# Kernel optimization log

Hardware: AMD Instinct MI355X
Metric: run time of the kernel (lower is better)

Reference implementation:

```python
import jax, jax.numpy as jnp
import numpy as np

SIZE = 4096  # core_size(16) ** nr_cores(3)


def setup_inputs() -> dict:
    key = jax.random.key(0)
    k_x, k0, k1, k2, kb = jax.random.split(key, 5)
    d, r = 16, 64
    # std per TT.init_core: sigma = (t * sqrt(r)**(1-c))**(1/c), t=1/sqrt(size), c=3
    t = 1.0 / np.sqrt(SIZE)
    sigma = float((t * np.sqrt(r) ** (1 - 3)) ** (1.0 / 3))
    x = jax.random.normal(k_x, (4, 2048, SIZE), dtype=jnp.float32)
    g0 = sigma * jax.random.normal(k0, (1, d, d, r), dtype=jnp.float32)
    g1 = sigma * jax.random.normal(k1, (r, d, d, r), dtype=jnp.float32)
    g2 = sigma * jax.random.normal(k2, (r, d, d, 1), dtype=jnp.float32)
    bias = np.sqrt(1.0 / SIZE) * jax.random.uniform(kb, (SIZE,), dtype=jnp.float32, minval=-1.0, maxval=1.0)
    return {"x": x, "g0": g0, "g1": g1, "g2": g2, "bias": bias}


def reference(x, g0, g1, g2, bias):
    # to_matrix: chain of einsum contractions over TT cores
    G = g0[0]  # (d, d, r)
    G = jnp.einsum('ija,aklb->ijklb', G, g1)      # (d,d,d,d,r)
    G = jnp.einsum('ijkla,amnb->ijklmnb', G, g2)  # (d,d,d,d,d,d,1)
    G = G.reshape(SIZE, SIZE)
    # forward: flatten leading dims, dense matmul + bias, restore shape
    X = x.reshape(-1, SIZE)
    out = X @ G + bias
    return out.reshape(*x.shape[:-1], SIZE)
```

## Files before the change

kernel.cpp:

```cpp
#include <hip/hip_runtime.h>
#include <stdint.h>

#define DI __device__ __forceinline__

using floatx4 = __attribute__((ext_vector_type(4))) float;
using short8  = __attribute__((ext_vector_type(8))) short;

DI uint16_t f2b(float f) {
  uint32_t u = __float_as_uint(f);
  return (uint16_t)((u + 0x7FFFu + ((u >> 16) & 1u)) >> 16);
}

DI void async_cp16(const uint16_t* g, uint16_t* l) {
  __builtin_amdgcn_global_load_lds(
      (const __attribute__((address_space(1))) void*)g,
      (__attribute__((address_space(3))) void*)l, 16, 0, 0);
}

__global__ __launch_bounds__(256)
void cvt_bf16(const float* __restrict__ x, uint16_t* __restrict__ y) {
  long i = ((long)blockIdx.x * 256 + threadIdx.x) * 8;
  float4 a = *(const float4*)(x + i);
  float4 b = *(const float4*)(x + i + 4);
  union { uint16_t u[8]; uint4 v; } o;
  o.u[0] = f2b(a.x); o.u[1] = f2b(a.y); o.u[2] = f2b(a.z); o.u[3] = f2b(a.w);
  o.u[4] = f2b(b.x); o.u[5] = f2b(b.y); o.u[6] = f2b(b.z); o.u[7] = f2b(b.w);
  *(uint4*)(y + i) = o.v;
}

__global__ __launch_bounds__(256)
void tt_t1(const float* __restrict__ g0, const float* __restrict__ g1,
           uint16_t* __restrict__ t1) {
  __shared__ float g0s[64 * 64];
  __shared__ float g1s[64 * 128];
  const int rowbase = blockIdx.x * 64;
  const int colbase = blockIdx.y * 128;
  const int t = threadIdx.x;

  for (int f = t; f < 4096; f += 256) g0s[f] = g0[rowbase * 64 + f];
  for (int f = t; f < 8192; f += 256) {
    int a = f >> 7, c = f & 127;
    g1s[f] = g1[(long)a * 16384 + colbase + c];
  }
  __syncthreads();

  const int tx = t & 31;
  const int ty = t >> 5;
  const int c0 = tx * 4;
  const int r0 = ty * 8;

  float acc[8][4];
  #pragma unroll
  for (int r = 0; r < 8; ++r)
    #pragma unroll
    for (int c = 0; c < 4; ++c) acc[r][c] = 0.f;

  for (int a4 = 0; a4 < 16; ++a4) {
    float g0r[8][4];
    #pragma unroll
    for (int r = 0; r < 8; ++r)
      *(float4*)&g0r[r][0] = *(const float4*)&g0s[(r0 + r) * 64 + a4 * 4];
    #pragma unroll
    for (int e = 0; e < 4; ++e) {
      float4 bv4 = *(const float4*)&g1s[(a4 * 4 + e) * 128 + c0];
      float bv[4] = {bv4.x, bv4.y, bv4.z, bv4.w};
      #pragma unroll
      for (int r = 0; r < 8; ++r)
        #pragma unroll
        for (int c = 0; c < 4; ++c)
          acc[r][c] += g0r[r][e] * bv[c];
    }
  }

  #pragma unroll
  for (int r = 0; r < 8; ++r) {
    ushort4 o;
    o.x = f2b(acc[r][0]); o.y = f2b(acc[r][1]);
    o.z = f2b(acc[r][2]); o.w = f2b(acc[r][3]);
    *(ushort4*)&t1[(long)(rowbase + r0 + r) * 16384 + colbase + c0] = o;
  }
}

__global__ __launch_bounds__(256)
void transpose_t1(const uint16_t* __restrict__ src, uint16_t* __restrict__ dst,
                  const float* __restrict__ g2, uint16_t* __restrict__ g2t) {
  __shared__ uint16_t tile[64][68];
  const int cb = blockIdx.x * 64;
  const int rb = blockIdx.y * 64;
  const int t = threadIdx.x;

  if (blockIdx.y == 0) {
    #pragma unroll
    for (int p = 0; p < 4; ++p) {
      int f = blockIdx.x * 1024 + p * 256 + t;
      int mn = f >> 6, b = f & 63;
      g2t[f] = f2b(g2[b * 256 + mn]);
    }
  }
  {
    const int c4 = (t & 15) * 4;
    const int r  = t >> 4;
    #pragma unroll
    for (int p = 0; p < 4; ++p) {
      int rr = r + p * 16;
      *(ushort4*)&tile[rr][c4] = *(const ushort4*)&src[(long)(rb + rr) * 1024 + cb + c4];
    }
  }
  __syncthreads();
  {
    const int r4 = (t & 15) * 4;
    const int c  = t >> 4;
    #pragma unroll
    for (int p = 0; p < 4; ++p) {
      int cc = c + p * 16;
      ushort4 o;
      o.x = tile[r4 + 0][cc]; o.y = tile[r4 + 1][cc];
      o.z = tile[r4 + 2][cc]; o.w = tile[r4 + 3][cc];
      *(ushort4*)&dst[(long)(cb + cc) * 4096 + rb + r4] = o;
    }
  }
}

#define VSTRIDE 136
__global__ __launch_bounds__(256, 2)
void gemm_fused(const uint16_t* __restrict__ A,
                const uint16_t* __restrict__ Bt,
                const uint16_t* __restrict__ g2t,
                const float* __restrict__ bias,
                float* __restrict__ out) {
  __shared__ __align__(16) uint16_t As[128 * 32];
  __shared__ __align__(16) uint16_t Bs[128 * 32];
  __shared__ __align__(16) uint16_t Vs[128 * VSTRIDE];

  const int bm = blockIdx.x * 128;
  const int bn = blockIdx.y * 128;
  const int tid  = threadIdx.x;
  const int wave = tid >> 6;
  const int lane = tid & 63;
  const int wm = (wave >> 1) * 64;
  const int wn = (wave & 1) * 64;

  const uint16_t* Ab = A + (long)bm * 4096;
  const uint16_t* Bb = Bt + (long)bn * 4096;

  const int srow = lane >> 2;
  const int scol = (lane & 3) * 8;

  floatx4 acc[4][4];
  #pragma unroll
  for (int i = 0; i < 4; ++i)
    #pragma unroll
    for (int j = 0; j < 4; ++j)
      acc[i][j] = (floatx4){0.f, 0.f, 0.f, 0.f};

  const int fr = lane & 15;
  const int fk = (lane >> 4) * 8;

  for (int k0 = 0; k0 < 4096; k0 += 32) {
    __syncthreads();
    #pragma unroll
    for (int t = 0; t < 2; ++t) {
      const int rblk = wave * 2 + t;
      async_cp16(Ab + (long)(rblk * 16 + srow) * 4096 + k0 + scol, &As[rblk * 16 * 32]);
      async_cp16(Bb + (long)(rblk * 16 + srow) * 4096 + k0 + scol, &Bs[rblk * 16 * 32]);
    }
    __syncthreads();

    short8 af[4], bg[4];
    #pragma unroll
    for (int i = 0; i < 4; ++i)
      af[i] = *(const short8*)&As[(wm + i * 16 + fr) * 32 + fk];
    #pragma unroll
    for (int j = 0; j < 4; ++j)
      bg[j] = *(const short8*)&Bs[(wn + j * 16 + fr) * 32 + fk];

    #pragma unroll
    for (int i = 0; i < 4; ++i)
      #pragma unroll
      for (int j = 0; j < 4; ++j)
        acc[i][j] = __builtin_amdgcn_mfma_f32_16x16x32_bf16(af[i], bg[j], acc[i][j], 0, 0, 0);
  }

  const int colq = lane & 15;
  const int rowq = (lane >> 4) * 4;
  __syncthreads();
  #pragma unroll
  for (int i = 0; i < 4; ++i)
    #pragma unroll
    for (int j = 0; j < 4; ++j)
      #pragma unroll
      for (int r = 0; r < 4; ++r)
        Vs[(wm + i * 16 + rowq + r) * VSTRIDE + wn + j * 16 + colq] = f2b(acc[i][j][r]);
  __syncthreads();

  const int bsel   = (wave >> 1) * 64;
  const int mnBase = (wave & 1) * 128;
  const long ocol0 = (long)blockIdx.y * 512 + (wave >> 1) * 256 + mnBase;

  short8 bg2[8][2];
  #pragma unroll
  for (int jn = 0; jn < 8; ++jn)
    #pragma unroll
    for (int ks = 0; ks < 2; ++ks)
      bg2[jn][ks] = *(const short8*)&g2t[(mnBase + jn * 16 + fr) * 64 + ks * 32 + fk];

  float bvs[8];
  #pragma unroll
  for (int jn = 0; jn < 8; ++jn)
    bvs[jn] = bias[ocol0 + jn * 16 + colq];

  #pragma unroll
  for (int pass = 0; pass < 4; ++pass) {
    floatx4 acc2[2][8];
    #pragma unroll
    for (int im = 0; im < 2; ++im)
      #pragma unroll
      for (int jn = 0; jn < 8; ++jn)
        acc2[im][jn] = (floatx4){0.f, 0.f, 0.f, 0.f};

    short8 af2[2][2];
    #pragma unroll
    for (int im = 0; im < 2; ++im)
      #pragma unroll
      for (int ks = 0; ks < 2; ++ks)
        af2[im][ks] = *(const short8*)&Vs[(pass * 32 + im * 16 + fr) * VSTRIDE + bsel + ks * 32 + fk];

    #pragma unroll
    for (int im = 0; im < 2; ++im)
      #pragma unroll
      for (int jn = 0; jn < 8; ++jn)
        #pragma unroll
        for (int ks = 0; ks < 2; ++ks)
          acc2[im][jn] = __builtin_amdgcn_mfma_f32_16x16x32_bf16(af2[im][ks], bg2[jn][ks], acc2[im][jn], 0, 0, 0);

    #pragma unroll
    for (int jn = 0; jn < 8; ++jn)
      #pragma unroll
      for (int im = 0; im < 2; ++im)
        #pragma unroll
        for (int r = 0; r < 4; ++r) {
          const int row = bm + pass * 32 + im * 16 + rowq + r;
          out[(long)row * 4096 + ocol0 + jn * 16 + colq] = acc2[im][jn][r] + bvs[jn];
        }
  }
}

static constexpr long XBF_OFF = 0;
static constexpr long T1_OFF  = 67108864;
static constexpr long T1T_OFF = 75497472;
static constexpr long G2T_OFF = 83886080;

extern "C" void kernel_launch(void* const* d_in, const int* in_sizes, int n_in,
                              void* d_out, int out_size, void* d_ws, size_t ws_size,
                              hipStream_t stream) {
  const float* x    = (const float*)d_in[0];
  const float* g0   = (const float*)d_in[1];
  const float* g1   = (const float*)d_in[2];
  const float* g2   = (const float*)d_in[3];
  const float* bias = (const float*)d_in[4];
  float* out = (float*)d_out;

  char* ws = (char*)d_ws;
  uint16_t* Xbf = (uint16_t*)(ws + XBF_OFF);
  uint16_t* T1  = (uint16_t*)(ws + T1_OFF);
  uint16_t* T1t = (uint16_t*)(ws + T1T_OFF);
  uint16_t* G2T = (uint16_t*)(ws + G2T_OFF);

  cvt_bf16<<<16384, 256, 0, stream>>>(x, Xbf);
  tt_t1<<<dim3(4, 128), 256, 0, stream>>>(g0, g1, T1);
  transpose_t1<<<dim3(16, 64), 256, 0, stream>>>(T1, T1t, g2, G2T);
  gemm_fused<<<dim3(64, 8), 256, 0, stream>>>(Xbf, T1t, G2T, bias, out);
}
```

Before: 350.6 us.

## Double-buffer GEMM mainloop with K=64 stages and a shared LDS pool

Rewrites the GEMM main loop to use two LDS buffers, each holding a K=64 slice of A and B. The async global-to-LDS copy for the next slice is issued before computing on the current one. This halves the number of barriers per K step and overlaps loads with MFMA work. The stage buffers and the epilogue V tile are aliased in one 64KB LDS array, which keeps LDS use near the original and may preserve two blocks per CU.

Result: faster. 335.0 us (-4.5%).

```diff
diff --git a/kernel.cpp b/kernel.cpp
--- a/kernel.cpp
+++ b/kernel.cpp
@@ -122,15 +122,46 @@
 }
 
 #define VSTRIDE 136
+
+DI void compute_half(const uint16_t* __restrict__ as_, const uint16_t* __restrict__ bs_,
+                     int wm, int wn, int fr, int fk, floatx4 acc[4][4]) {
+  short8 af[4], bg[4];
+  #pragma unroll
+  for (int i = 0; i < 4; ++i)
+    af[i] = *(const short8*)&as_[(wm + i * 16 + fr) * 32 + fk];
+  #pragma unroll
+  for (int j = 0; j < 4; ++j)
+    bg[j] = *(const short8*)&bs_[(wn + j * 16 + fr) * 32 + fk];
+  #pragma unroll
+  for (int i = 0; i < 4; ++i)
+    #pragma unroll
+    for (int j = 0; j < 4; ++j)
+      acc[i][j] = __builtin_amdgcn_mfma_f32_16x16x32_bf16(af[i], bg[j], acc[i][j], 0, 0, 0);
+}
+
+DI void stage_tile(const uint16_t* __restrict__ Ab, const uint16_t* __restrict__ Bb,
+                   uint16_t* dstbuf, int k0, int wave, int srow, int scol) {
+  #pragma unroll
+  for (int ks = 0; ks < 2; ++ks)
+    #pragma unroll
+    for (int t = 0; t < 2; ++t) {
+      const int rblk = wave * 2 + t;
+      async_cp16(Ab + (long)(rblk * 16 + srow) * 4096 + k0 + ks * 32 + scol,
+                 dstbuf + ks * 4096 + rblk * 16 * 32);
+      async_cp16(Bb + (long)(rblk * 16 + srow) * 4096 + k0 + ks * 32 + scol,
+                 dstbuf + 8192 + ks * 4096 + rblk * 16 * 32);
+    }
+}
+
 __global__ __launch_bounds__(256, 2)
 void gemm_fused(const uint16_t* __restrict__ A,
                 const uint16_t* __restrict__ Bt,
                 const uint16_t* __restrict__ g2t,
                 const float* __restrict__ bias,
                 float* __restrict__ out) {
-  __shared__ __align__(16) uint16_t As[128 * 32];
-  __shared__ __align__(16) uint16_t Bs[128 * 32];
-  __shared__ __align__(16) uint16_t Vs[128 * VSTRIDE];
+  __shared__ __align__(16) uint16_t lds[32768];
+  uint16_t* buf0 = lds;
+  uint16_t* buf1 = lds + 16384;
 
   const int bm = blockIdx.x * 128;
   const int bn = blockIdx.y * 128;
@@ -145,6 +176,8 @@
 
   const int srow = lane >> 2;
   const int scol = (lane & 3) * 8;
+  const int fr = lane & 15;
+  const int fk = (lane >> 4) * 8;
 
   floatx4 acc[4][4];
   #pragma unroll
@@ -153,33 +186,26 @@
     for (int j = 0; j < 4; ++j)
       acc[i][j] = (floatx4){0.f, 0.f, 0.f, 0.f};
 
-  const int fr = lane & 15;
-  const int fk = (lane >> 4) * 8;
-
-  for (int k0 = 0; k0 < 4096; k0 += 32) {
+  stage_tile(Ab, Bb, buf0, 0, wave, srow, scol);
+  __syncthreads();
+
+  for (int t = 0; t < 62; t += 2) {
+    stage_tile(Ab, Bb, buf1, (t + 1) * 64, wave, srow, scol);
+    compute_half(buf0,        buf0 + 8192,  wm, wn, fr, fk, acc);
+    compute_half(buf0 + 4096, buf0 + 12288, wm, wn, fr, fk, acc);
     __syncthreads();
-    #pragma unroll
-    for (int t = 0; t < 2; ++t) {
-      const int rblk = wave * 2 + t;
-      async_cp16(Ab + (long)(rblk * 16 + srow) * 4096 + k0 + scol, &As[rblk * 16 * 32]);
-      async_cp16(Bb + (long)(rblk * 16 + srow) * 4096 + k0 + scol, &Bs[rblk * 16 * 32]);
-    }
+
+    stage_tile(Ab, Bb, buf0, (t + 2) * 64, wave, srow, scol);
+    compute_half(buf1,        buf1 + 8192,  wm, wn, fr, fk, acc);
+    compute_half(buf1 + 4096, buf1 + 12288, wm, wn, fr, fk, acc);
     __syncthreads();
-
-    short8 af[4], bg[4];
-    #pragma unroll
-    for (int i = 0; i < 4; ++i)
-      af[i] = *(const short8*)&As[(wm + i * 16 + fr) * 32 + fk];
-    #pragma unroll
-    for (int j = 0; j < 4; ++j)
-      bg[j] = *(const short8*)&Bs[(wn + j * 16 + fr) * 32 + fk];
-
-    #pragma unroll
-    for (int i = 0; i < 4; ++i)
-      #pragma unroll
-      for (int j = 0; j < 4; ++j)
-        acc[i][j] = __builtin_amdgcn_mfma_f32_16x16x32_bf16(af[i], bg[j], acc[i][j], 0, 0, 0);
-  }
+  }
+  stage_tile(Ab, Bb, buf1, 63 * 64, wave, srow, scol);
+  compute_half(buf0,        buf0 + 8192,  wm, wn, fr, fk, acc);
+  compute_half(buf0 + 4096, buf0 + 12288, wm, wn, fr, fk, acc);
+  __syncthreads();
+  compute_half(buf1,        buf1 + 8192,  wm, wn, fr, fk, acc);
+  compute_half(buf1 + 4096, buf1 + 12288, wm, wn, fr, fk, acc);
 
   const int colq = lane & 15;
   const int rowq = (lane >> 4) * 4;
@@ -190,7 +216,7 @@
     for (int j = 0; j < 4; ++j)
       #pragma unroll
       for (int r = 0; r < 4; ++r)
-        Vs[(wm + i * 16 + rowq + r) * VSTRIDE + wn + j * 16 + colq] = f2b(acc[i][j][r]);
+        lds[(wm + i * 16 + rowq + r) * VSTRIDE + wn + j * 16 + colq] = f2b(acc[i][j][r]);
   __syncthreads();
 
   const int bsel   = (wave >> 1) * 64;
@@ -223,7 +249,7 @@
     for (int im = 0; im < 2; ++im)
       #pragma unroll
       for (int ks = 0; ks < 2; ++ks)
-        af2[im][ks] = *(const short8*)&Vs[(pass * 32 + im * 16 + fr) * VSTRIDE + bsel + ks * 32 + fk];
+        af2[im][ks] = *(const short8*)&lds[(pass * 32 + im * 16 + fr) * VSTRIDE + bsel + ks * 32 + fk];
 
     #pragma unroll
     for (int im = 0; im < 2; ++im)
```

## Rewrite fused GEMM with 256x128 tiles, triple-buffered async loads and swizzled LDS

Applied to the files above, without the earlier changes.

The main GEMM now uses 512-thread blocks covering 256x128 output tiles with K-steps of 64. Operands are loaded into LDS through a three-buffer async pipeline, using an XOR swizzle to avoid bank conflicts. MFMA work is split into quads interleaved with prefetch, barriers and setprio. The epilogue also uses the swizzled layout, with 8 waves each computing a 64-column slice of the second contraction. This aims to hide global-load latency behind compute and reduce per-iteration barrier stalls, at the cost of about 144KB of dynamic LDS and higher register pressure, which limits occupancy.

New measurement: 339.6 us. -3.1%, faster.

```diff
diff --git a/kernel.cpp b/kernel.cpp
--- a/kernel.cpp
+++ b/kernel.cpp
@@ -121,30 +121,66 @@
   }
 }
 
-#define VSTRIDE 136
-__global__ __launch_bounds__(256, 2)
+#define LDSA 16384
+#define BUFS 24576
+
+DI short8 ld_frag(const uint16_t* buf, int row, int c) {
+  return *(const short8*)&buf[row * 64 + ((c ^ (row & 7)) << 3)];
+}
+
+DI void stageA2(const uint16_t* Ab, uint16_t* Abuf, int k0,
+                int wave, int srow, int schunk8, int q0) {
+  #pragma unroll
+  for (int q = 0; q < 2; ++q) {
+    const int rblk = wave * 4 + q0 + q;
+    async_cp16(Ab + (long)(rblk * 8 + srow) * 4096 + k0 + schunk8,
+               Abuf + rblk * 512);
+  }
+}
+
+DI void stageB2(const uint16_t* Bb, uint16_t* Bbuf, int k0,
+                int wave, int srow, int schunk8) {
+  #pragma unroll
+  for (int q = 0; q < 2; ++q) {
+    const int rblk = wave * 2 + q;
+    async_cp16(Bb + (long)(rblk * 8 + srow) * 4096 + k0 + schunk8,
+               Bbuf + rblk * 512);
+  }
+}
+
+#define MFMA_QUAD(I0, J0)                                                    \
+  _Pragma("unroll")                                                          \
+  for (int i_ = 0; i_ < 2; ++i_)                                             \
+    _Pragma("unroll")                                                        \
+    for (int j_ = 0; j_ < 2; ++j_)                                           \
+      _Pragma("unroll")                                                      \
+      for (int ks_ = 0; ks_ < 2; ++ks_)                                      \
+        acc[(I0) + i_][(J0) + j_] = __builtin_amdgcn_mfma_f32_16x16x32_bf16( \
+            af[(I0) + i_][ks_], bg[(J0) + j_][ks_], acc[(I0) + i_][(J0) + j_], 0, 0, 0);
+
+__global__ __launch_bounds__(512, 2)
 void gemm_fused(const uint16_t* __restrict__ A,
                 const uint16_t* __restrict__ Bt,
                 const uint16_t* __restrict__ g2t,
                 const float* __restrict__ bias,
                 float* __restrict__ out) {
-  __shared__ __align__(16) uint16_t As[128 * 32];
-  __shared__ __align__(16) uint16_t Bs[128 * 32];
-  __shared__ __align__(16) uint16_t Vs[128 * VSTRIDE];
-
-  const int bm = blockIdx.x * 128;
-  const int bn = blockIdx.y * 128;
+  extern __shared__ uint16_t lds[];
+
+  const int bm = blockIdx.x * 256;
+  const int by = blockIdx.y;
   const int tid  = threadIdx.x;
   const int wave = tid >> 6;
   const int lane = tid & 63;
   const int wm = (wave >> 1) * 64;
   const int wn = (wave & 1) * 64;
-
-  const uint16_t* Ab = A + (long)bm * 4096;
-  const uint16_t* Bb = Bt + (long)bn * 4096;
-
-  const int srow = lane >> 2;
-  const int scol = (lane & 3) * 8;
+  const int fr = lane & 15;
+  const int ck = lane >> 4;
+
+  const int srow    = lane >> 3;
+  const int schunk8 = (((lane & 7) ^ srow) << 3);
+
+  const uint16_t* Ab = A  + (long)bm * 4096;
+  const uint16_t* Bb = Bt + (long)by * 128 * 4096;
 
   floatx4 acc[4][4];
   #pragma unroll
@@ -153,93 +189,139 @@
     for (int j = 0; j < 4; ++j)
       acc[i][j] = (floatx4){0.f, 0.f, 0.f, 0.f};
 
-  const int fr = lane & 15;
-  const int fk = (lane >> 4) * 8;
-
-  for (int k0 = 0; k0 < 4096; k0 += 32) {
-    __syncthreads();
-    #pragma unroll
-    for (int t = 0; t < 2; ++t) {
-      const int rblk = wave * 2 + t;
-      async_cp16(Ab + (long)(rblk * 16 + srow) * 4096 + k0 + scol, &As[rblk * 16 * 32]);
-      async_cp16(Bb + (long)(rblk * 16 + srow) * 4096 + k0 + scol, &Bs[rblk * 16 * 32]);
-    }
-    __syncthreads();
-
-    short8 af[4], bg[4];
-    #pragma unroll
-    for (int i = 0; i < 4; ++i)
-      af[i] = *(const short8*)&As[(wm + i * 16 + fr) * 32 + fk];
-    #pragma unroll
-    for (int j = 0; j < 4; ++j)
-      bg[j] = *(const short8*)&Bs[(wn + j * 16 + fr) * 32 + fk];
-
-    #pragma unroll
-    for (int i = 0; i < 4; ++i)
-      #pragma unroll
-      for (int j = 0; j < 4; ++j)
-        acc[i][j] = __builtin_amdgcn_mfma_f32_16x16x32_bf16(af[i], bg[j], acc[i][j], 0, 0, 0);
+  uint16_t* pc = lds;
+  uint16_t* pn = lds + BUFS;
+  uint16_t* ps = lds + 2 * BUFS;
+
+  stageA2(Ab, pc, 0, wave, srow, schunk8, 0);
+  stageA2(Ab, pc, 0, wave, srow, schunk8, 2);
+  stageB2(Bb, pc + LDSA, 0, wave, srow, schunk8);
+  stageA2(Ab, pn, 64, wave, srow, schunk8, 0);
+  stageA2(Ab, pn, 64, wave, srow, schunk8, 2);
+  stageB2(Bb, pn + LDSA, 64, wave, srow, schunk8);
+  asm volatile("s_waitcnt vmcnt(6)" ::: "memory");
+  __builtin_amdgcn_s_barrier();
+
+  for (int t = 0; t < 64; ++t) {
+    const int k2 = (t + 2) * 64;
+    const bool pf = (t < 62);
+    short8 af[4][2], bg[4][2];
+
+    #pragma unroll
+    for (int x = 0; x < 2; ++x)
+      #pragma unroll
+      for (int ks = 0; ks < 2; ++ks) {
+        af[x][ks] = ld_frag(pc,        wm + x * 16 + fr, ks * 4 + ck);
+        bg[x][ks] = ld_frag(pc + LDSA, wn + x * 16 + fr, ks * 4 + ck);
+      }
+    if (pf) stageA2(Ab, ps, k2, wave, srow, schunk8, 0);
+    __builtin_amdgcn_s_barrier();
+    __builtin_amdgcn_s_setprio(1);
+    MFMA_QUAD(0, 0);
+    __builtin_amdgcn_s_setprio(0);
+    __builtin_amdgcn_s_barrier();
+
+    #pragma unroll
+    for (int x = 2; x < 4; ++x)
+      #pragma unroll
+      for (int ks = 0; ks < 2; ++ks)
+        bg[x][ks] = ld_frag(pc + LDSA, wn + x * 16 + fr, ks * 4 + ck);
+    if (pf) stageA2(Ab, ps, k2, wave, srow, schunk8, 2);
+    __builtin_amdgcn_s_barrier();
+    __builtin_amdgcn_s_setprio(1);
+    MFMA_QUAD(0, 2);
+    __builtin_amdgcn_s_setprio(0);
+    __builtin_amdgcn_s_barrier();
+
+    #pragma unroll
+    for (int x = 2; x < 4; ++x)
+      #pragma unroll
+      for (int ks = 0; ks < 2; ++ks)
+        af[x][ks] = ld_frag(pc, wm + x * 16 + fr, ks * 4 + ck);
+    if (pf) stageB2(Bb, ps + LDSA, k2, wave, srow, schunk8);
+    __builtin_amdgcn_s_barrier();
+    __builtin_amdgcn_s_setprio(1);
+    MFMA_QUAD(2, 2);
+    __builtin_amdgcn_s_setprio(0);
+    __builtin_amdgcn_s_barrier();
+
+    __builtin_amdgcn_s_setprio(1);
+    MFMA_QUAD(2, 0);
+    __builtin_amdgcn_s_setprio(0);
+    if (t < 62) asm volatile("s_waitcnt vmcnt(6)" ::: "memory");
+    else        asm volatile("s_waitcnt vmcnt(0)" ::: "memory");
+    __builtin_amdgcn_s_barrier();
+
+    uint16_t* tmp = pc; pc = pn; pn = ps; ps = tmp;
   }
 
   const int colq = lane & 15;
   const int rowq = (lane >> 4) * 4;
+  #pragma unroll
+  for (int i = 0; i < 4; ++i)
+    #pragma unroll
+    for (int j = 0; j < 4; ++j)
+      #pragma unroll
+      for (int r = 0; r < 4; ++r) {
+        const int row = wm + i * 16 + rowq + r;
+        const int col = wn + j * 16 + colq;
+        const int pos = ((col >> 3) & 8) | (((col >> 3) & 7) ^ (row & 7));
+        lds[row * 128 + pos * 8 + (col & 7)] = f2b(acc[i][j][r]);
+      }
   __syncthreads();
-  #pragma unroll
-  for (int i = 0; i < 4; ++i)
-    #pragma unroll
-    for (int j = 0; j < 4; ++j)
-      #pragma unroll
-      for (int r = 0; r < 4; ++r)
-        Vs[(wm + i * 16 + rowq + r) * VSTRIDE + wn + j * 16 + colq] = f2b(acc[i][j][r]);
-  __syncthreads();
-
-  const int bsel   = (wave >> 1) * 64;
-  const int mnBase = (wave & 1) * 128;
-  const long ocol0 = (long)blockIdx.y * 512 + (wave >> 1) * 256 + mnBase;
-
-  short8 bg2[8][2];
-  #pragma unroll
-  for (int jn = 0; jn < 8; ++jn)
+
+  const int lsel   = wave >> 2;
+  const int mnBase = (wave & 3) * 64;
+  const long ocol0 = (long)by * 512 + lsel * 256 + mnBase;
+  const int fk = ck * 8;
+
+  short8 bg2[4][2];
+  #pragma unroll
+  for (int jn = 0; jn < 4; ++jn)
     #pragma unroll
     for (int ks = 0; ks < 2; ++ks)
       bg2[jn][ks] = *(const short8*)&g2t[(mnBase + jn * 16 + fr) * 64 + ks * 32 + fk];
 
-  float bvs[8];
-  #pragma unroll
-  for (int jn = 0; jn < 8; ++jn)
+  float bvs[4];
+  #pragma unroll
+  for (int jn = 0; jn < 4; ++jn)
     bvs[jn] = bias[ocol0 + jn * 16 + colq];
 
   #pragma unroll
   for (int pass = 0; pass < 4; ++pass) {
-    floatx4 acc2[2][8];
-    #pragma unroll
-    for (int im = 0; im < 2; ++im)
-      #pragma unroll
-      for (int jn = 0; jn < 8; ++jn)
+    floatx4 acc2[4][4];
+    #pragma unroll
+    for (int im = 0; im < 4; ++im)
+      #pragma unroll
+      for (int jn = 0; jn < 4; ++jn)
         acc2[im][jn] = (floatx4){0.f, 0.f, 0.f, 0.f};
 
-    short8 af2[2][2];
-    #pragma unroll
-    for (int im = 0; im < 2; ++im)
-      #pragma unroll
-      for (int ks = 0; ks < 2; ++ks)
-        af2[im][ks] = *(const short8*)&Vs[(pass * 32 + im * 16 + fr) * VSTRIDE + bsel + ks * 32 + fk];
-
-    #pragma unroll
-    for (int im = 0; im < 2; ++im)
-      #pragma unroll
-      for (int jn = 0; jn < 8; ++jn)
+    short8 af2[4][2];
+    #pragma unroll
+    for (int im = 0; im < 4; ++im)
+      #pragma unroll
+      for (int ks = 0; ks < 2; ++ks) {
+        const int row = pass * 64 + im * 16 + fr;
+        af2[im][ks] = *(const short8*)&lds[row * 128 +
+                        ((lsel * 8 + ((ks * 4 + ck) ^ (row & 7))) << 3)];
+      }
+
+    #pragma unroll
+    for (int im = 0; im < 4; ++im)
+      #pragma unroll
+      for (int jn = 0; jn < 4; ++jn)
         #pragma unroll
         for (int ks = 0; ks < 2; ++ks)
-          acc2[im][jn] = __builtin_amdgcn_mfma_f32_16x16x32_bf16(af2[im][ks], bg2[jn][ks], acc2[im][jn], 0, 0, 0);
-
-    #pragma unroll
-    for (int jn = 0; jn < 8; ++jn)
-      #pragma unroll
-      for (int im = 0; im < 2; ++im)
+          acc2[im][jn] = __builtin_amdgcn_mfma_f32_16x16x32_bf16(
+              af2[im][ks], bg2[jn][ks], acc2[im][jn], 0, 0, 0);
+
+    #pragma unroll
+    for (int jn = 0; jn < 4; ++jn)
+      #pragma unroll
+      for (int im = 0; im < 4; ++im)
         #pragma unroll
         for (int r = 0; r < 4; ++r) {
-          const int row = bm + pass * 32 + im * 16 + rowq + r;
+          const int row = bm + pass * 64 + im * 16 + rowq + r;
           out[(long)row * 4096 + ocol0 + jn * 16 + colq] = acc2[im][jn][r] + bvs[jn];
         }
   }
@@ -266,8 +348,11 @@
   uint16_t* T1t = (uint16_t*)(ws + T1T_OFF);
   uint16_t* G2T = (uint16_t*)(ws + G2T_OFF);
 
+  hipFuncSetAttribute((const void*)gemm_fused,
+                      hipFuncAttributeMaxDynamicSharedMemorySize, 3 * BUFS * 2);
+
   cvt_bf16<<<16384, 256, 0, stream>>>(x, Xbf);
   tt_t1<<<dim3(4, 128), 256, 0, stream>>>(g0, g1, T1);
   transpose_t1<<<dim3(16, 64), 256, 0, stream>>>(T1, T1t, g2, G2T);
-  gemm_fused<<<dim3(64, 8), 256, 0, stream>>>(Xbf, T1t, G2T, bias, out);
-}
+  gemm_fused<<<dim3(32, 8), 512, 3 * BUFS * 2, stream>>>(Xbf, T1t, G2T, bias, out);
+}
```
